# Kernel optimization log

Hardware: AMD Instinct MI355X
Metric: run time of the kernel (lower is better)

## Reference

```python
import jax, jax.numpy as jnp
import numpy as np

N_NODES = 100000
N_EDGES = 1000000
IN_DIM = 64
OUT_DIM = 64
BN_EPS = 1e-5


def setup_inputs() -> dict:
    key = jax.random.key(0)
    k1, k2, k3 = jax.random.split(key, 3)
    x = jax.random.normal(k1, (N_NODES, IN_DIM), dtype=jnp.float32)
    edge_index = jax.random.randint(k2, (2, N_EDGES), 0, N_NODES, dtype=jnp.int32)
    W = jax.random.normal(k3, (IN_DIM, OUT_DIM), dtype=jnp.float32) * (1.0 / np.sqrt(IN_DIM))
    b = jnp.zeros((OUT_DIM,), dtype=jnp.float32)
    gamma = jnp.ones((OUT_DIM,), dtype=jnp.float32)
    beta = jnp.zeros((OUT_DIM,), dtype=jnp.float32)
    return {"x": x, "edge_index": edge_index, "W": W, "b": b, "gamma": gamma, "beta": beta}


def reference(x, edge_index, W, b, gamma, beta):
    N = x.shape[0]
    # GCN normalization with self-loops (improved=False -> fill value 1.0)
    loop = jnp.arange(N, dtype=edge_index.dtype)
    src = jnp.concatenate([edge_index[0], loop])  # message sources
    dst = jnp.concatenate([edge_index[1], loop])  # aggregation targets
    ew = jnp.ones(src.shape[0], dtype=x.dtype)
    deg = jax.ops.segment_sum(ew, dst, num_segments=N)  # [N]
    dinv = jnp.where(deg > 0, jax.lax.rsqrt(deg), 0.0)
    norm = dinv[src] * ew * dinv[dst]  # [E+N]
    # linear transform then normalized scatter-add aggregation
    h = x @ W  # [N, OUT_DIM]
    msg = h[src] * norm[:, None]  # [E+N, OUT_DIM]
    agg = jax.ops.segment_sum(msg, dst, num_segments=N) + b  # [N, OUT_DIM]
    # activation
    a = jax.nn.relu(agg)
    # BatchNorm1d, training mode: batch statistics over node dim (biased var)
    mean = jnp.mean(a, axis=0)
    var = jnp.mean((a - mean) ** 2, axis=0)
    out = gamma * (a - mean) * jax.lax.rsqrt(var + BN_EPS) + beta
    return out
```

## Files before the change

kernel.cpp:

```cpp
#include <hip/hip_runtime.h>
#include <hip/hip_fp16.h>

#define DIM 64
#define BN_EPS 1e-5f
#define RSHIFT 8
#define RSIZE 256
#define EPB 8192
#define ABLK 2048
#define RBLK 128
#define BH 512

__global__ __launch_bounds__(256) void k_binhist(const int* __restrict__ dst,
                                                 int* __restrict__ bhist,
                                                 int P, int E) {
    __shared__ int hist[BH];
    for (int b0 = threadIdx.x; b0 < BH; b0 += 256) hist[b0] = 0;
    __syncthreads();
    const int base4 = blockIdx.x * (EPB / 4);
    for (int i = 0; i < EPB / 4 / 256; ++i) {
        int idx = base4 + i * 256 + threadIdx.x;
        int e0 = idx << 2;
        if (e0 + 3 < E) {
            int4 d4 = ((const int4*)dst)[idx];
            atomicAdd(&hist[d4.x >> RSHIFT], 1);
            atomicAdd(&hist[d4.y >> RSHIFT], 1);
            atomicAdd(&hist[d4.z >> RSHIFT], 1);
            atomicAdd(&hist[d4.w >> RSHIFT], 1);
        } else {
            for (int k = 0; k < 4; ++k)
                if (e0 + k < E) atomicAdd(&hist[dst[e0 + k] >> RSHIFT], 1);
        }
    }
    __syncthreads();
    for (int b0 = threadIdx.x; b0 < P; b0 += 256)
        bhist[blockIdx.x * BH + b0] = hist[b0];
}

__global__ __launch_bounds__(128) void k_binscan(int* __restrict__ bhist,
                                                 int* __restrict__ bintot,
                                                 int nbin) {
    __shared__ int s[128];
    const int r = blockIdx.x;
    int carry = 0;
    for (int base = 0; base < nbin; base += 128) {
        const int idx = base + threadIdx.x;
        int v = (idx < nbin) ? bhist[idx * BH + r] : 0;
        s[threadIdx.x] = v;
        __syncthreads();
        for (int off = 1; off < 128; off <<= 1) {
            int t = (threadIdx.x >= (unsigned)off) ? s[threadIdx.x - off] : 0;
            __syncthreads();
            s[threadIdx.x] += t;
            __syncthreads();
        }
        if (idx < nbin) bhist[idx * BH + r] = carry + s[threadIdx.x] - v;
        carry += s[127];
        __syncthreads();
    }
    if (threadIdx.x == 0) bintot[r] = carry;
}

__global__ void k_gscan(const int* __restrict__ bintot, int* __restrict__ gbase,
                        int* __restrict__ rowptr, int P, int N, int E) {
    __shared__ int s[512];
    int v = ((int)threadIdx.x < P) ? bintot[threadIdx.x] : 0;
    s[threadIdx.x] = v;
    __syncthreads();
    for (int off = 1; off < 512; off <<= 1) {
        int t = (threadIdx.x >= (unsigned)off) ? s[threadIdx.x - off] : 0;
        __syncthreads();
        s[threadIdx.x] += t;
        __syncthreads();
    }
    if ((int)threadIdx.x < P) gbase[threadIdx.x] = s[threadIdx.x] - v;
    if ((int)threadIdx.x == P - 1) gbase[P] = s[threadIdx.x];
    if (threadIdx.x == 0) rowptr[N] = E;
}

__global__ __launch_bounds__(256) void k_bin(const int* __restrict__ src,
                                             const int* __restrict__ dst,
                                             const int* __restrict__ gbase,
                                             const int* __restrict__ bhist,
                                             int* __restrict__ pk, int P, int E) {
    __shared__ int gofs[BH], lcnt[BH];
    for (int b0 = threadIdx.x; b0 < P; b0 += 256) {
        gofs[b0] = gbase[b0] + bhist[blockIdx.x * BH + b0];
        lcnt[b0] = 0;
    }
    __syncthreads();
    const int base4 = blockIdx.x * (EPB / 4);
    for (int i = 0; i < EPB / 4 / 256; ++i) {
        int idx = base4 + i * 256 + threadIdx.x;
        int e0 = idx << 2;
        if (e0 + 3 < E) {
            int4 d4 = ((const int4*)dst)[idx];
            int4 s4 = ((const int4*)src)[idx];
            int b0;
            b0 = d4.x >> RSHIFT; pk[gofs[b0] + atomicAdd(&lcnt[b0], 1)] = ((d4.x & (RSIZE - 1)) << 20) | s4.x;
            b0 = d4.y >> RSHIFT; pk[gofs[b0] + atomicAdd(&lcnt[b0], 1)] = ((d4.y & (RSIZE - 1)) << 20) | s4.y;
            b0 = d4.z >> RSHIFT; pk[gofs[b0] + atomicAdd(&lcnt[b0], 1)] = ((d4.z & (RSIZE - 1)) << 20) | s4.z;
            b0 = d4.w >> RSHIFT; pk[gofs[b0] + atomicAdd(&lcnt[b0], 1)] = ((d4.w & (RSIZE - 1)) << 20) | s4.w;
        } else {
            for (int k = 0; k < 4; ++k) {
                if (e0 + k < E) {
                    int d = dst[e0 + k];
                    int b0 = d >> RSHIFT;
                    pk[gofs[b0] + atomicAdd(&lcnt[b0], 1)] = ((d & (RSIZE - 1)) << 20) | src[e0 + k];
                }
            }
        }
    }
}

__global__ __launch_bounds__(256) void k_sortrange(
        const int* __restrict__ gbase, const int* __restrict__ pk,
        int* __restrict__ ssrc, int* __restrict__ rowptr,
        float* __restrict__ dinv, int N) {
    __shared__ int lhist[256], ls[256], lcur[256];
    const int r = blockIdx.x;
    const int d0 = r << RSHIFT;
    const int i = d0 + threadIdx.x;
    const int ebeg = gbase[r], eend = gbase[r + 1];
    lhist[threadIdx.x] = 0;
    __syncthreads();
    for (int j = ebeg + threadIdx.x; j < eend; j += 256)
        atomicAdd(&lhist[((unsigned)pk[j]) >> 20], 1);
    __syncthreads();
    int dg = lhist[threadIdx.x];
    if (i < N) dinv[i] = rsqrtf((float)dg + 1.0f);
    ls[threadIdx.x] = dg;
    __syncthreads();
    for (int off = 1; off < 256; off <<= 1) {
        int t = (threadIdx.x >= (unsigned)off) ? ls[threadIdx.x - off] : 0;
        __syncthreads();
        ls[threadIdx.x] += t;
        __syncthreads();
    }
    int lofs = ls[threadIdx.x] - dg;
    lcur[threadIdx.x] = ebeg + lofs;
    if (i < N) rowptr[i] = ebeg + lofs;
    __syncthreads();
    for (int j = ebeg + threadIdx.x; j < eend; j += 256) {
        int p = pk[j];
        ssrc[atomicAdd(&lcur[((unsigned)p) >> 20], 1)] = p & 0xFFFFF;
    }
}

__global__ __launch_bounds__(256) void k_gemm(const float* __restrict__ x,
                                              const float* __restrict__ W,
                                              const float* __restrict__ dinv,
                                              __half* __restrict__ h2, int N) {
    __shared__ float Wl[DIM * DIM];
    for (int i = threadIdx.x; i < DIM * DIM; i += 256) Wl[i] = W[i];
    __syncthreads();
    int t = blockIdx.x * 256 + threadIdx.x;
    int r = t >> 2;
    int q = t & 3;
    if (r >= N) return;
    const float4* xr4 = (const float4*)(x + (size_t)r * DIM);
    float4 acc[4];
#pragma unroll
    for (int j = 0; j < 4; ++j) acc[j] = make_float4(0.f, 0.f, 0.f, 0.f);
    for (int k0 = 0; k0 < 16; ++k0) {
        float4 xv = xr4[k0];
#pragma unroll
        for (int kk = 0; kk < 4; ++kk) {
            float xs = (&xv.x)[kk];
            const float4* wrow = (const float4*)(Wl + (k0 * 4 + kk) * DIM) + (q << 2);
#pragma unroll
            for (int j = 0; j < 4; ++j) {
                float4 w = wrow[j];
                acc[j].x += xs * w.x;
                acc[j].y += xs * w.y;
                acc[j].z += xs * w.z;
                acc[j].w += xs * w.w;
            }
        }
    }
    float dr = dinv[r];
    float4* hr4 = (float4*)(h2 + (size_t)r * DIM) + (q << 1);
    union { __half2 h[4]; float4 f4; } pack;
#pragma unroll
    for (int j = 0; j < 4; j += 2) {
        pack.h[0] = __float22half2_rn(make_float2(acc[j].x * dr, acc[j].y * dr));
        pack.h[1] = __float22half2_rn(make_float2(acc[j].z * dr, acc[j].w * dr));
        pack.h[2] = __float22half2_rn(make_float2(acc[j + 1].x * dr, acc[j + 1].y * dr));
        pack.h[3] = __float22half2_rn(make_float2(acc[j + 1].z * dr, acc[j + 1].w * dr));
        hr4[j >> 1] = pack.f4;
    }
}

__global__ __launch_bounds__(256) void k_nodeagg(
        const int* __restrict__ rowptr, const int* __restrict__ ssrc,
        const __half* __restrict__ h2, const float* __restrict__ dinv,
        const float* __restrict__ b, __half* __restrict__ a2,
        float* __restrict__ pstats, int N) {
    const int lane = threadIdx.x & 63;
    const int w = threadIdx.x >> 6;
    const float bl = b[lane];
    const __half* hb = h2 + lane;
    float psum = 0.f, psq = 0.f;
    const int npairs = N >> 1;
    for (int t = blockIdx.x * 4 + w; t < npairs; t += ABLK * 4) {
        const int i0 = t << 1;
        const int rb0 = rowptr[i0], rb1 = rowptr[i0 + 1], rb2 = rowptr[i0 + 2];
        float acc0 = __half2float(hb[(size_t)i0 * DIM]);
        float acc1 = __half2float(hb[(size_t)(i0 + 1) * DIM]);
        const int total = rb2 - rb0;
        for (int j0 = 0; j0 < total; j0 += 64) {
            const int m = min(64, total - j0);
            const int c = rb1 - rb0 - j0;
            int sv = ssrc[rb0 + j0 + min(lane, m - 1)];
            int j = 0;
            for (; j + 16 <= m; j += 16) {
                int sA[16];
                float vA[16];
#pragma unroll
                for (int k = 0; k < 16; ++k) sA[k] = __builtin_amdgcn_readlane(sv, j + k);
#pragma unroll
                for (int k = 0; k < 16; ++k) vA[k] = __half2float(hb[(size_t)sA[k] * DIM]);
#pragma unroll
                for (int k = 0; k < 16; ++k) {
                    if (j + k < c) acc0 += vA[k]; else acc1 += vA[k];
                }
            }
            if (j < m) {
                const int r = m - j;
                int sA[16];
                float vA[16];
#pragma unroll
                for (int k = 0; k < 16; ++k) sA[k] = __builtin_amdgcn_readlane(sv, j + min(k, r - 1));
#pragma unroll
                for (int k = 0; k < 16; ++k) vA[k] = __half2float(hb[(size_t)sA[k] * DIM]);
#pragma unroll
                for (int k = 0; k < 16; ++k) {
                    if (k < r) { if (j + k < c) acc0 += vA[k]; else acc1 += vA[k]; }
                }
            }
        }
        float a0 = fmaxf(acc0 * dinv[i0] + bl, 0.f);
        float a1 = fmaxf(acc1 * dinv[i0 + 1] + bl, 0.f);
        a2[(size_t)i0 * DIM + lane] = __float2half_rn(a0);
        a2[(size_t)(i0 + 1) * DIM + lane] = __float2half_rn(a1);
        psum += a0 + a1;
        psq += a0 * a0 + a1 * a1;
    }
    __shared__ float s1[256], s2[256];
    s1[threadIdx.x] = psum;
    s2[threadIdx.x] = psq;
    __syncthreads();
    if (threadIdx.x < 128) {
        s1[threadIdx.x] += s1[threadIdx.x + 128];
        s2[threadIdx.x] += s2[threadIdx.x + 128];
    }
    __syncthreads();
    if (threadIdx.x < 64) {
        pstats[(size_t)blockIdx.x * 128 + threadIdx.x] = s1[threadIdx.x] + s1[threadIdx.x + 64];
        pstats[(size_t)blockIdx.x * 128 + 64 + threadIdx.x] = s2[threadIdx.x] + s2[threadIdx.x + 64];
    }
}

__global__ __launch_bounds__(128) void k_redstats(const float* __restrict__ pstats,
                                                  float* __restrict__ pstats2) {
    const int f = threadIdx.x;
    const size_t base = (size_t)blockIdx.x * (ABLK / RBLK) * 128;
    float s = 0.f;
#pragma unroll 8
    for (int j = 0; j < ABLK / RBLK; ++j)
        s += pstats[base + (size_t)j * 128 + f];
    pstats2[(size_t)blockIdx.x * 128 + f] = s;
}

__global__ void k_finstats(const float* __restrict__ pstats2,
                           const float* __restrict__ gamma, const float* __restrict__ beta,
                           float* __restrict__ scale, float* __restrict__ shift, int N) {
    __shared__ float ssum[1024], ssq[1024];
    const int f = threadIdx.x & 63;
    const int c = threadIdx.x >> 6;
    float s = 0.f, q = 0.f;
    for (int blk = c; blk < RBLK; blk += 16) {
        s += pstats2[blk * 128 + f];
        q += pstats2[blk * 128 + 64 + f];
    }
    ssum[threadIdx.x] = s;
    ssq[threadIdx.x] = q;
    __syncthreads();
    for (int o = 512; o >= 64; o >>= 1) {
        if ((int)threadIdx.x < o) {
            ssum[threadIdx.x] += ssum[threadIdx.x + o];
            ssq[threadIdx.x] += ssq[threadIdx.x + o];
        }
        __syncthreads();
    }
    if (threadIdx.x < 64) {
        float inv_n = 1.0f / (float)N;
        float mean = ssum[f] * inv_n;
        float var = ssq[f] * inv_n - mean * mean;
        float istd = rsqrtf(var + BN_EPS);
        float sc = gamma[f] * istd;
        scale[f] = sc;
        shift[f] = beta[f] - mean * sc;
    }
}

__global__ void k_bn2(const __half* __restrict__ a2, const float* __restrict__ scale,
                      const float* __restrict__ shift, float* __restrict__ out, int total8) {
    int i = blockIdx.x * blockDim.x + threadIdx.x;
    const int stride = gridDim.x * blockDim.x;
    const int f8 = i & 7;
    const float4 sc0 = ((const float4*)scale)[f8 * 2];
    const float4 sc1 = ((const float4*)scale)[f8 * 2 + 1];
    const float4 sh0 = ((const float4*)shift)[f8 * 2];
    const float4 sh1 = ((const float4*)shift)[f8 * 2 + 1];
    for (; i < total8; i += stride) {
        union { float4 f; __half2 h[4]; } u;
        u.f = ((const float4*)a2)[i];
        float2 p0 = __half22float2(u.h[0]);
        float2 p1 = __half22float2(u.h[1]);
        float2 p2 = __half22float2(u.h[2]);
        float2 p3 = __half22float2(u.h[3]);
        float4 o0 = make_float4(p0.x * sc0.x + sh0.x, p0.y * sc0.y + sh0.y,
                                p1.x * sc0.z + sh0.z, p1.y * sc0.w + sh0.w);
        float4 o1 = make_float4(p2.x * sc1.x + sh1.x, p2.y * sc1.y + sh1.y,
                                p3.x * sc1.z + sh1.z, p3.y * sc1.w + sh1.w);
        ((float4*)out)[(size_t)i * 2] = o0;
        ((float4*)out)[(size_t)i * 2 + 1] = o1;
    }
}

extern "C" void kernel_launch(void* const* d_in, const int* in_sizes, int n_in,
                              void* d_out, int out_size, void* d_ws, size_t ws_size,
                              hipStream_t stream) {
    const float* x     = (const float*)d_in[0];
    const int*   ei    = (const int*)d_in[1];
    const float* W     = (const float*)d_in[2];
    const float* b     = (const float*)d_in[3];
    const float* gamma = (const float*)d_in[4];
    const float* beta  = (const float*)d_in[5];
    float* out = (float*)d_out;

    const int N = in_sizes[0] / DIM;
    const int E = in_sizes[1] / 2;
    const int* esrc = ei;
    const int* edst = ei + E;
    const int P = (N + RSIZE - 1) >> RSHIFT;
    const int nbin = (E + EPB - 1) / EPB;

    char* ws = (char*)d_ws;
    size_t off = 0;
    int* bhist = (int*)(ws + off);      off += (size_t)nbin * BH * sizeof(int);
    off = (off + 255) & ~(size_t)255;
    int* bintot = (int*)(ws + off);     off += 512 * sizeof(int);
    int* gbase = (int*)(ws + off);      off += 520 * sizeof(int);
    off = (off + 255) & ~(size_t)255;
    float* dinv = (float*)(ws + off);   off += (size_t)N * sizeof(float);
    off = (off + 255) & ~(size_t)255;
    int* rowptr = (int*)(ws + off);     off += (size_t)(N + 1) * sizeof(int);
    off = (off + 255) & ~(size_t)255;
    float* scale = (float*)(ws + off);  off += 64 * sizeof(float);
    float* shift = (float*)(ws + off);  off += 64 * sizeof(float);
    off = (off + 255) & ~(size_t)255;
    float* pstats = (float*)(ws + off); off += (size_t)ABLK * 128 * sizeof(float);
    off = (off + 255) & ~(size_t)255;
    float* pstats2 = (float*)(ws + off); off += (size_t)RBLK * 128 * sizeof(float);
    off = (off + 255) & ~(size_t)255;
    int* pk = (int*)(ws + off);         off += (size_t)E * sizeof(int);
    off = (off + 255) & ~(size_t)255;
    int* ssrc = (int*)(ws + off);       off += (size_t)E * sizeof(int);
    off = (off + 255) & ~(size_t)255;
    __half* h2 = (__half*)(ws + off);   off += (size_t)N * DIM * sizeof(__half);
    off = (off + 255) & ~(size_t)255;
    __half* a2 = (__half*)(ws + off);   off += (size_t)N * DIM * sizeof(__half);

    k_binhist<<<nbin, 256, 0, stream>>>(edst, bhist, P, E);
    k_binscan<<<P, 128, 0, stream>>>(bhist, bintot, nbin);
    k_gscan<<<1, 512, 0, stream>>>(bintot, gbase, rowptr, P, N, E);
    k_bin<<<nbin, 256, 0, stream>>>(esrc, edst, gbase, bhist, pk, P, E);
    k_sortrange<<<P, 256, 0, stream>>>(gbase, pk, ssrc, rowptr, dinv, N);
    k_gemm<<<(4 * N + 255) / 256, 256, 0, stream>>>(x, W, dinv, h2, N);
    k_nodeagg<<<ABLK, 256, 0, stream>>>(rowptr, ssrc, h2, dinv, b, a2, pstats, N);
    k_redstats<<<RBLK, 128, 0, stream>>>(pstats, pstats2);
    k_finstats<<<1, 1024, 0, stream>>>(pstats2, gamma, beta, scale, shift, N);
    k_bn2<<<1024, 256, 0, stream>>>(a2, scale, shift, out, N * DIM / 8);
}
```

Measured before the change: 184.4 us.

## Fold small scan and stats-reduction kernels into neighbours to cut launches

Merges the global bin scan into k_binscan using a last-block-done atomic counter, so the single-block gscan launch goes away. The per-block BN statistics are accumulated with atomics into 16 slots, zeroed inside k_gemm, instead of being written per block and reduced by two extra kernels. Each k_bn2 block now finalises scale and shift itself from the slots. This removes three kernel launches and their serial gaps, at the cost of atomic contention, nondeterministic float summation order, and redundant finalisation work in every bn2 block.

```diff
diff --git a/kernel.cpp b/kernel.cpp
--- a/kernel.cpp
+++ b/kernel.cpp
@@ -7,12 +7,14 @@
 #define RSIZE 256
 #define EPB 8192
 #define ABLK 2048
-#define RBLK 128
+#define PSLOT 16
 #define BH 512
 
 __global__ __launch_bounds__(256) void k_binhist(const int* __restrict__ dst,
                                                  int* __restrict__ bhist,
+                                                 int* __restrict__ donecnt,
                                                  int P, int E) {
+    if (blockIdx.x == 0 && threadIdx.x == 0) *donecnt = 0;
     __shared__ int hist[BH];
     for (int b0 = threadIdx.x; b0 < BH; b0 += 256) hist[b0] = 0;
     __syncthreads();
@@ -38,8 +40,12 @@
 
 __global__ __launch_bounds__(128) void k_binscan(int* __restrict__ bhist,
                                                  int* __restrict__ bintot,
-                                                 int nbin) {
+                                                 int* __restrict__ gbase,
+                                                 int* __restrict__ rowptr,
+                                                 int* __restrict__ donecnt,
+                                                 int P, int N, int E, int nbin) {
     __shared__ int s[128];
+    __shared__ int lastflag;
     const int r = blockIdx.x;
     int carry = 0;
     for (int base = 0; base < nbin; base += 128) {
@@ -57,24 +63,34 @@
         carry += s[127];
         __syncthreads();
     }
-    if (threadIdx.x == 0) bintot[r] = carry;
-}
-
-__global__ void k_gscan(const int* __restrict__ bintot, int* __restrict__ gbase,
-                        int* __restrict__ rowptr, int P, int N, int E) {
-    __shared__ int s[512];
-    int v = ((int)threadIdx.x < P) ? bintot[threadIdx.x] : 0;
-    s[threadIdx.x] = v;
-    __syncthreads();
-    for (int off = 1; off < 512; off <<= 1) {
-        int t = (threadIdx.x >= (unsigned)off) ? s[threadIdx.x - off] : 0;
-        __syncthreads();
-        s[threadIdx.x] += t;
-        __syncthreads();
-    }
-    if ((int)threadIdx.x < P) gbase[threadIdx.x] = s[threadIdx.x] - v;
-    if ((int)threadIdx.x == P - 1) gbase[P] = s[threadIdx.x];
-    if (threadIdx.x == 0) rowptr[N] = E;
+    if (threadIdx.x == 0) {
+        bintot[r] = carry;
+        __threadfence();
+        int prev = atomicAdd(donecnt, 1);
+        lastflag = (prev == (int)gridDim.x - 1);
+    }
+    __syncthreads();
+    if (!lastflag) return;
+    int carry2 = 0;
+    for (int base = 0; base < P; base += 128) {
+        const int idx = base + threadIdx.x;
+        int v = (idx < P) ? atomicAdd(&bintot[idx], 0) : 0;
+        s[threadIdx.x] = v;
+        __syncthreads();
+        for (int off = 1; off < 128; off <<= 1) {
+            int t = (threadIdx.x >= (unsigned)off) ? s[threadIdx.x - off] : 0;
+            __syncthreads();
+            s[threadIdx.x] += t;
+            __syncthreads();
+        }
+        if (idx < P) gbase[idx] = carry2 + s[threadIdx.x] - v;
+        carry2 += s[127];
+        __syncthreads();
+    }
+    if (threadIdx.x == 0) {
+        gbase[P] = carry2;
+        rowptr[N] = E;
+    }
 }
 
 __global__ __launch_bounds__(256) void k_bin(const int* __restrict__ src,
@@ -149,7 +165,11 @@
 __global__ __launch_bounds__(256) void k_gemm(const float* __restrict__ x,
                                               const float* __restrict__ W,
                                               const float* __restrict__ dinv,
-                                              __half* __restrict__ h2, int N) {
+                                              __half* __restrict__ h2,
+                                              float* __restrict__ pstats2, int N) {
+    if (blockIdx.x == 0) {
+        for (int i = threadIdx.x; i < PSLOT * 128; i += 256) pstats2[i] = 0.f;
+    }
     __shared__ float Wl[DIM * DIM];
     for (int i = threadIdx.x; i < DIM * DIM; i += 256) Wl[i] = W[i];
     __syncthreads();
@@ -194,7 +214,7 @@
         const int* __restrict__ rowptr, const int* __restrict__ ssrc,
         const __half* __restrict__ h2, const float* __restrict__ dinv,
         const float* __restrict__ b, __half* __restrict__ a2,
-        float* __restrict__ pstats, int N) {
+        float* __restrict__ pstats2, int N) {
     const int lane = threadIdx.x & 63;
     const int w = threadIdx.x >> 6;
     const float bl = b[lane];
@@ -255,63 +275,43 @@
     }
     __syncthreads();
     if (threadIdx.x < 64) {
-        pstats[(size_t)blockIdx.x * 128 + threadIdx.x] = s1[threadIdx.x] + s1[threadIdx.x + 64];
-        pstats[(size_t)blockIdx.x * 128 + 64 + threadIdx.x] = s2[threadIdx.x] + s2[threadIdx.x + 64];
-    }
-}
-
-__global__ __launch_bounds__(128) void k_redstats(const float* __restrict__ pstats,
-                                                  float* __restrict__ pstats2) {
-    const int f = threadIdx.x;
-    const size_t base = (size_t)blockIdx.x * (ABLK / RBLK) * 128;
-    float s = 0.f;
-#pragma unroll 8
-    for (int j = 0; j < ABLK / RBLK; ++j)
-        s += pstats[base + (size_t)j * 128 + f];
-    pstats2[(size_t)blockIdx.x * 128 + f] = s;
-}
-
-__global__ void k_finstats(const float* __restrict__ pstats2,
-                           const float* __restrict__ gamma, const float* __restrict__ beta,
-                           float* __restrict__ scale, float* __restrict__ shift, int N) {
-    __shared__ float ssum[1024], ssq[1024];
-    const int f = threadIdx.x & 63;
-    const int c = threadIdx.x >> 6;
-    float s = 0.f, q = 0.f;
-    for (int blk = c; blk < RBLK; blk += 16) {
-        s += pstats2[blk * 128 + f];
-        q += pstats2[blk * 128 + 64 + f];
-    }
-    ssum[threadIdx.x] = s;
-    ssq[threadIdx.x] = q;
-    __syncthreads();
-    for (int o = 512; o >= 64; o >>= 1) {
-        if ((int)threadIdx.x < o) {
-            ssum[threadIdx.x] += ssum[threadIdx.x + o];
-            ssq[threadIdx.x] += ssq[threadIdx.x + o];
-        }
-        __syncthreads();
-    }
+        const int slot = (blockIdx.x & (PSLOT - 1)) * 128;
+        atomicAdd(&pstats2[slot + threadIdx.x], s1[threadIdx.x] + s1[threadIdx.x + 64]);
+        atomicAdd(&pstats2[slot + 64 + threadIdx.x], s2[threadIdx.x] + s2[threadIdx.x + 64]);
+    }
+}
+
+__global__ __launch_bounds__(256) void k_bn2(const __half* __restrict__ a2,
+                                             const float* __restrict__ pstats2,
+                                             const float* __restrict__ gamma,
+                                             const float* __restrict__ beta,
+                                             float* __restrict__ out, int total8, int N) {
+    __shared__ float ssc[64], ssh[64];
+    if (threadIdx.x < 128) {
+        float s = 0.f;
+#pragma unroll
+        for (int k = 0; k < PSLOT; ++k) s += pstats2[k * 128 + threadIdx.x];
+        if (threadIdx.x < 64) ssc[threadIdx.x] = s;
+        else ssh[threadIdx.x - 64] = s;
+    }
+    __syncthreads();
     if (threadIdx.x < 64) {
         float inv_n = 1.0f / (float)N;
-        float mean = ssum[f] * inv_n;
-        float var = ssq[f] * inv_n - mean * mean;
+        float mean = ssc[threadIdx.x] * inv_n;
+        float var = ssh[threadIdx.x] * inv_n - mean * mean;
         float istd = rsqrtf(var + BN_EPS);
-        float sc = gamma[f] * istd;
-        scale[f] = sc;
-        shift[f] = beta[f] - mean * sc;
-    }
-}
-
-__global__ void k_bn2(const __half* __restrict__ a2, const float* __restrict__ scale,
-                      const float* __restrict__ shift, float* __restrict__ out, int total8) {
+        float sc = gamma[threadIdx.x] * istd;
+        ssc[threadIdx.x] = sc;
+        ssh[threadIdx.x] = beta[threadIdx.x] - mean * sc;
+    }
+    __syncthreads();
     int i = blockIdx.x * blockDim.x + threadIdx.x;
     const int stride = gridDim.x * blockDim.x;
     const int f8 = i & 7;
-    const float4 sc0 = ((const float4*)scale)[f8 * 2];
-    const float4 sc1 = ((const float4*)scale)[f8 * 2 + 1];
-    const float4 sh0 = ((const float4*)shift)[f8 * 2];
-    const float4 sh1 = ((const float4*)shift)[f8 * 2 + 1];
+    const float4 sc0 = ((const float4*)ssc)[f8 * 2];
+    const float4 sc1 = ((const float4*)ssc)[f8 * 2 + 1];
+    const float4 sh0 = ((const float4*)ssh)[f8 * 2];
+    const float4 sh1 = ((const float4*)ssh)[f8 * 2 + 1];
     for (; i < total8; i += stride) {
         union { float4 f; __half2 h[4]; } u;
         u.f = ((const float4*)a2)[i];
@@ -353,16 +353,13 @@
     int* bintot = (int*)(ws + off);     off += 512 * sizeof(int);
     int* gbase = (int*)(ws + off);      off += 520 * sizeof(int);
     off = (off + 255) & ~(size_t)255;
+    int* donecnt = (int*)(ws + off);    off += 256;
+    off = (off + 255) & ~(size_t)255;
     float* dinv = (float*)(ws + off);   off += (size_t)N * sizeof(float);
     off = (off + 255) & ~(size_t)255;
     int* rowptr = (int*)(ws + off);     off += (size_t)(N + 1) * sizeof(int);
     off = (off + 255) & ~(size_t)255;
-    float* scale = (float*)(ws + off);  off += 64 * sizeof(float);
-    float* shift = (float*)(ws + off);  off += 64 * sizeof(float);
-    off = (off + 255) & ~(size_t)255;
-    float* pstats = (float*)(ws + off); off += (size_t)ABLK * 128 * sizeof(float);
-    off = (off + 255) & ~(size_t)255;
-    float* pstats2 = (float*)(ws + off); off += (size_t)RBLK * 128 * sizeof(float);
+    float* pstats2 = (float*)(ws + off); off += (size_t)PSLOT * 128 * sizeof(float);
     off = (off + 255) & ~(size_t)255;
     int* pk = (int*)(ws + off);         off += (size_t)E * sizeof(int);
     off = (off + 255) & ~(size_t)255;
@@ -372,14 +369,11 @@
     off = (off + 255) & ~(size_t)255;
     __half* a2 = (__half*)(ws + off);   off += (size_t)N * DIM * sizeof(__half);
 
-    k_binhist<<<nbin, 256, 0, stream>>>(edst, bhist, P, E);
-    k_binscan<<<P, 128, 0, stream>>>(bhist, bintot, nbin);
-    k_gscan<<<1, 512, 0, stream>>>(bintot, gbase, rowptr, P, N, E);
+    k_binhist<<<nbin, 256, 0, stream>>>(edst, bhist, donecnt, P, E);
+    k_binscan<<<P, 128, 0, stream>>>(bhist, bintot, gbase, rowptr, donecnt, P, N, E, nbin);
     k_bin<<<nbin, 256, 0, stream>>>(esrc, edst, gbase, bhist, pk, P, E);
     k_sortrange<<<P, 256, 0, stream>>>(gbase, pk, ssrc, rowptr, dinv, N);
-    k_gemm<<<(4 * N + 255) / 256, 256, 0, stream>>>(x, W, dinv, h2, N);
-    k_nodeagg<<<ABLK, 256, 0, stream>>>(rowptr, ssrc, h2, dinv, b, a2, pstats, N);
-    k_redstats<<<RBLK, 128, 0, stream>>>(pstats, pstats2);
-    k_finstats<<<1, 1024, 0, stream>>>(pstats2, gamma, beta, scale, shift, N);
-    k_bn2<<<1024, 256, 0, stream>>>(a2, scale, shift, out, N * DIM / 8);
-}
+    k_gemm<<<(4 * N + 255) / 256, 256, 0, stream>>>(x, W, dinv, h2, pstats2, N);
+    k_nodeagg<<<ABLK, 256, 0, stream>>>(rowptr, ssrc, h2, dinv, b, a2, pstats2, N);
+    k_bn2<<<1024, 256, 0, stream>>>(a2, pstats2, gamma, beta, out, N * DIM / 8, N);
+}
```

Result: slower. 192.2 us (+4.2%).
